# Kernel tuning notes

Hardware: AMD Instinct MI355X
Metric: run time of the kernel (lower is better)

The kernel has to match this reference:

```python
import jax, jax.numpy as jnp
import numpy as np
from jax import lax

DIM = 384
HEADS = 8
HEAD_DIM = DIM // HEADS  # 48
GROUPS = 2               # GKVA num_group
MLP_DIM = 4 * DIM
EPS = 1e-5


def _layernorm(x, g, b):
    m = jnp.mean(x, axis=-1, keepdims=True)
    v = jnp.var(x, axis=-1, keepdims=True)
    return (x - m) * lax.rsqrt(v + EPS) * g + b


def _cpe(x, w, b, dims):
    # depthwise Conv3d positional encoding; x: (B,N,C)
    B, N, C = x.shape
    D, H, W = dims
    feat = jnp.transpose(x.reshape(B, D, H, W, C), (0, 4, 1, 2, 3))  # (B,C,D,H,W)
    feat = lax.conv_general_dilated(
        feat, w, (1, 1, 1), 'SAME',
        dimension_numbers=('NCDHW', 'OIDHW', 'NCDHW'),
        feature_group_count=C)
    feat = feat + b[None, :, None, None, None]
    feat = jnp.transpose(feat, (0, 2, 3, 4, 1)).reshape(B, N, C)
    return x + feat


def _channel_attn_gkva(x, q_w, kv_w, proj_w, proj_b):
    # x: (B,N,C). GKVA: q has num_group heads, kv has full num_heads split into groups.
    B, N, C = x.shape
    scale = HEAD_DIM ** -0.5
    hpg = HEADS // GROUPS  # heads per group = 4
    q = (x @ q_w).reshape(B, 1, N, GROUPS, HEAD_DIM)
    q = jnp.transpose(q, (0, 3, 1, 2, 4))                 # (B,G,1,N,hd)
    kv = (x @ kv_w).reshape(B, N, 2, GROUPS, hpg, HEAD_DIM)
    kv = jnp.transpose(kv, (2, 0, 3, 4, 1, 5))            # (2,B,G,hpg,N,hd)
    k, v = kv[0] * scale, kv[1]
    # channel attention: (hd x hd) score per head, softmax in fp32
    att = jnp.einsum('bghnc,bghnd->bghcd', k, v)          # (B,G,hpg,hd,hd)
    att = jax.nn.softmax(att.astype(jnp.float32), axis=-1).astype(x.dtype)
    y = att @ jnp.swapaxes(q, -1, -2)                     # (B,G,hpg,hd,N) via broadcast over hpg
    y = jnp.swapaxes(y, -1, -2)                           # (B,G,hpg,N,hd)
    y = jnp.transpose(y, (0, 2, 1, 3, 4)).reshape(B, N, C)  # faithful to torch transpose(1,2).reshape
    return y @ proj_w + proj_b


def reference(x, attn_mask, cpe0_w, cpe0_b, cpe1_w, cpe1_b,
              norm1_g, norm1_b, q_w, kv_w, proj_w, proj_b,
              norm2_g, norm2_b, mlp_w1, mlp_b1, mlp_w2, mlp_b2):
    B, D, H, W, C = x.shape
    dims = (D, H, W)
    xf = x.reshape(B, -1, C)
    xf = _cpe(xf, cpe0_w, cpe0_b, dims)
    cur = _channel_attn_gkva(_layernorm(xf, norm1_g, norm1_b), q_w, kv_w, proj_w, proj_b)
    xf = xf + cur  # drop_path = 0 -> identity
    xf = _cpe(xf, cpe1_w, cpe1_b, dims)
    h = _layernorm(xf, norm2_g, norm2_b)
    h = jax.nn.gelu(h @ mlp_w1 + mlp_b1, approximate=False) @ mlp_w2 + mlp_b2
    xf = xf + h
    return xf.reshape(B, D, H, W, C)


def setup_inputs() -> dict:
    key = jax.random.key(0)
    ks = jax.random.split(key, 16)
    B, D, H, W, C = 4, 8, 32, 32, DIM
    s = 0.02
    inp = {
        'x': jax.random.normal(ks[0], (B, D, H, W, C), jnp.float32),
        'attn_mask': jnp.zeros((1, 343, 343), jnp.float32),
        'cpe0_w': jax.random.normal(ks[1], (C, 1, 3, 3, 3), jnp.float32) * s,
        'cpe0_b': jnp.zeros((C,), jnp.float32),
        'cpe1_w': jax.random.normal(ks[2], (C, 1, 3, 3, 3), jnp.float32) * s,
        'cpe1_b': jnp.zeros((C,), jnp.float32),
        'norm1_g': jnp.ones((C,), jnp.float32),
        'norm1_b': jnp.zeros((C,), jnp.float32),
        'q_w': jax.random.normal(ks[3], (C, HEAD_DIM * GROUPS), jnp.float32) * s,
        'kv_w': jax.random.normal(ks[4], (C, 2 * C), jnp.float32) * s,
        'proj_w': jax.random.normal(ks[5], (C, C), jnp.float32) * s,
        'proj_b': jnp.zeros((C,), jnp.float32),
        'norm2_g': jnp.ones((C,), jnp.float32),
        'norm2_b': jnp.zeros((C,), jnp.float32),
        'mlp_w1': jax.random.normal(ks[6], (C, MLP_DIM), jnp.float32) * s,
        'mlp_b1': jnp.zeros((MLP_DIM,), jnp.float32),
        'mlp_w2': jax.random.normal(ks[7], (MLP_DIM, C), jnp.float32) * s,
        'mlp_b2': jnp.zeros((C,), jnp.float32),
    }
    return inp
```

## Files before the change

### kernel.cpp

```cpp
#include <hip/hip_runtime.h>
#include <hip/hip_bf16.h>
#include <math.h>

using bf16 = __hip_bfloat16;
typedef __attribute__((ext_vector_type(8))) short s16x8;
typedef __attribute__((ext_vector_type(4))) float f32x4;

__device__ __forceinline__ float bf2f(unsigned short u) {
    return __uint_as_float(((unsigned int)u) << 16);
}
__device__ __forceinline__ unsigned short f2bf(float f) {
    union { bf16 b; unsigned short u; } cv; cv.b = __float2bfloat16(f); return cv.u;
}
__device__ __forceinline__ float4 ld4(const float* p) { return *(const float4*)p; }
__device__ __forceinline__ float4 ld4(const bf16* p) {
    ushort4 u = *(const ushort4*)p;
    return make_float4(bf2f(u.x), bf2f(u.y), bf2f(u.z), bf2f(u.w));
}

#define GLD16(g, l) __builtin_amdgcn_global_load_lds( \
    (const __attribute__((address_space(1))) unsigned int*)(const void*)(g), \
    (__attribute__((address_space(3))) unsigned int*)(void*)(l), 16, 0, 0)

__device__ __forceinline__ void wtbT(const float* __restrict__ src,
                                     bf16* __restrict__ dst, int K, int N, int i)
{
    int n = i / K, k = i % K;
    dst[i] = (n < N) ? __float2bfloat16(src[k * N + n]) : __float2bfloat16(0.f);
}

__global__ __launch_bounds__(256) void prep_kernel(
    const float* q_w, const float* kv_w, const float* proj_w,
    const float* w1, const float* w2,
    const float* cpe0_w, const float* cpe1_w,
    bf16* qwT, bf16* kvwT, bf16* pwT, bf16* w1T, bf16* w2T,
    float* wt0, float* wt1)
{
    int i = blockIdx.x * 256 + threadIdx.x;
    if      (i < 49152)   wtbT(q_w,    qwT,  384, 96,   i);
    else if (i < 344064)  wtbT(kv_w,   kvwT, 384, 768,  i - 49152);
    else if (i < 491520)  wtbT(proj_w, pwT,  384, 384,  i - 344064);
    else if (i < 1081344) wtbT(w1,     w1T,  384, 1536, i - 491520);
    else if (i < 1671168) wtbT(w2,     w2T,  1536, 384, i - 1081344);
    else if (i < 1681536) { int j = i - 1671168; wt0[(j % 27) * 384 + j / 27] = cpe0_w[j]; }
    else if (i < 1691904) { int j = i - 1681536; wt1[(j % 27) * 384 + j / 27] = cpe1_w[j]; }
}

template <typename T>
__global__ __launch_bounds__(384) void cpe_ln_kernel(
    const T* __restrict__ src, const float* __restrict__ wgtT,
    const float* __restrict__ bias, const float* __restrict__ gam,
    const float* __restrict__ bet, bf16* __restrict__ xf_out,
    bf16* __restrict__ t_out)
{
    const int tid = threadIdx.x;
    const int qd = tid % 96, c = qd * 4;
    const int wseg = tid / 96, w_base = wseg * 8;
    const int blk = blockIdx.x;
    const int h = blk & 31, d = (blk >> 5) & 7, b = blk >> 8;

    const float4 bv = *(const float4*)(bias + c);
    float4 acc[8];
    #pragma unroll
    for (int o = 0; o < 8; ++o) acc[o] = bv;

    #pragma unroll
    for (int kd = 0; kd < 3; ++kd) {
        const int dd = d + kd - 1;
        if ((unsigned)dd >= 8u) continue;
        #pragma unroll
        for (int kh = 0; kh < 3; ++kh) {
            const int hh = h + kh - 1;
            if ((unsigned)hh >= 32u) continue;
            const int tap0 = kd * 9 + kh * 3;
            const float4 w0 = *(const float4*)(wgtT + (tap0 + 0) * 384 + c);
            const float4 w1 = *(const float4*)(wgtT + (tap0 + 1) * 384 + c);
            const float4 w2 = *(const float4*)(wgtT + (tap0 + 2) * 384 + c);
            const T* rowp = src + ((((size_t)b * 8 + dd) * 32 + hh) * 32) * 384 + c;
            #pragma unroll
            for (int p = 0; p < 10; ++p) {
                const int ww = w_base + p - 1;
                const float m = ((unsigned)ww < 32u) ? 1.f : 0.f;
                const int wwc = min(max(ww, 0), 31);
                float4 sv = ld4(rowp + (size_t)wwc * 384);
                sv.x *= m; sv.y *= m; sv.z *= m; sv.w *= m;
                if (p < 8) {
                    acc[p].x += sv.x * w0.x; acc[p].y += sv.y * w0.y;
                    acc[p].z += sv.z * w0.z; acc[p].w += sv.w * w0.w;
                }
                if (p >= 1 && p <= 8) {
                    acc[p-1].x += sv.x * w1.x; acc[p-1].y += sv.y * w1.y;
                    acc[p-1].z += sv.z * w1.z; acc[p-1].w += sv.w * w1.w;
                }
                if (p >= 2) {
                    acc[p-2].x += sv.x * w2.x; acc[p-2].y += sv.y * w2.y;
                    acc[p-2].z += sv.z * w2.z; acc[p-2].w += sv.w * w2.w;
                }
            }
        }
    }
    const size_t rowoff = ((((size_t)b * 8 + d) * 32 + h) * 32) * 384 + c;
    float4 r[8];
    __shared__ float2 part[32][96];
    #pragma unroll
    for (int o = 0; o < 8; ++o) {
        const size_t off = rowoff + (size_t)(w_base + o) * 384;
        const float4 s0 = ld4(src + off);
        r[o].x = s0.x + acc[o].x; r[o].y = s0.y + acc[o].y;
        r[o].z = s0.z + acc[o].z; r[o].w = s0.w + acc[o].w;
        ushort4 u;
        u.x = f2bf(r[o].x); u.y = f2bf(r[o].y); u.z = f2bf(r[o].z); u.w = f2bf(r[o].w);
        *(ushort4*)((unsigned short*)xf_out + off) = u;
        const float s = r[o].x + r[o].y + r[o].z + r[o].w;
        const float s2 = r[o].x*r[o].x + r[o].y*r[o].y + r[o].z*r[o].z + r[o].w*r[o].w;
        part[w_base + o][qd] = make_float2(s, s2);
    }
    __syncthreads();
    __shared__ float2 red[32][12];
    {
        const int tk = tid / 12, j = tid % 12;
        float s = 0.f, s2 = 0.f;
        #pragma unroll
        for (int u = 0; u < 8; ++u) {
            const float2 p = part[tk][j * 8 + u];
            s += p.x; s2 += p.y;
        }
        red[tk][j] = make_float2(s, s2);
    }
    __syncthreads();
    __shared__ float2 stats[32];
    if (tid < 32) {
        float s = 0.f, s2 = 0.f;
        #pragma unroll
        for (int j = 0; j < 12; ++j) { s += red[tid][j].x; s2 += red[tid][j].y; }
        const float mean = s * (1.f / 384.f);
        const float var = s2 * (1.f / 384.f) - mean * mean;
        stats[tid] = make_float2(mean, rsqrtf(var + 1e-5f));
    }
    __syncthreads();
    const float4 gv = *(const float4*)(gam + c);
    const float4 be = *(const float4*)(bet + c);
    #pragma unroll
    for (int o = 0; o < 8; ++o) {
        const int tk = w_base + o;
        const float2 st = stats[tk];
        ushort4 u;
        u.x = f2bf((r[o].x - st.x) * st.y * gv.x + be.x);
        u.y = f2bf((r[o].y - st.x) * st.y * gv.y + be.y);
        u.z = f2bf((r[o].z - st.x) * st.y * gv.z + be.z);
        u.w = f2bf((r[o].w - st.x) * st.y * gv.w + be.w);
        *(ushort4*)((unsigned short*)t_out + (size_t)(blk * 32 + tk) * 384 + c) = u;
    }
}

__global__ __launch_bounds__(256) void gemm128_kernel(
    const bf16* __restrict__ A, int lda,
    const bf16* __restrict__ BT, int ldb,
    void* outp, int ldo, const void* resp, const float* __restrict__ bias,
    int Nout, int K, int flags)
{
    __shared__ unsigned short As[128 * 64];
    __shared__ unsigned short Bs[128 * 64];
    const int tid = threadIdx.x;
    const int wid = tid >> 6, lane = tid & 63;
    const int m0 = blockIdx.y * 128, n0 = blockIdx.x * 128;
    const int moff = (wid >> 1) * 64, noff = (wid & 1) * 64;
    const int lrow = lane & 15, quad = lane >> 4;
    const int srow = lane >> 3;
    const int scol = ((lane & 7) ^ srow) * 8;
    const int sw = lrow & 7;

    f32x4 acc[4][4] = {};

    for (int k0 = 0; k0 < K; k0 += 64) {
        #pragma unroll
        for (int j = 0; j < 4; ++j) {
            const int r = (wid * 4 + j) * 8 + srow;
            GLD16(A + (size_t)(m0 + r) * lda + k0 + scol, As + (wid * 4 + j) * 512);
        }
        #pragma unroll
        for (int j = 0; j < 4; ++j) {
            const int r = (wid * 4 + j) * 8 + srow;
            GLD16(BT + (size_t)(n0 + r) * ldb + k0 + scol, Bs + (wid * 4 + j) * 512);
        }
        __syncthreads();
        #pragma unroll
        for (int ks = 0; ks < 64; ks += 32) {
            const int kc = (ks >> 3) + quad;
            const int koff = ((kc ^ sw) << 3);
            s16x8 af[4], bfr[4];
            #pragma unroll
            for (int i = 0; i < 4; ++i)
                af[i] = *(const s16x8*)(As + (moff + i * 16 + lrow) * 64 + koff);
            #pragma unroll
            for (int i = 0; i < 4; ++i)
                bfr[i] = *(const s16x8*)(Bs + (noff + i * 16 + lrow) * 64 + koff);
            #pragma unroll
            for (int mi = 0; mi < 4; ++mi)
                #pragma unroll
                for (int ni = 0; ni < 4; ++ni)
                    acc[mi][ni] = __builtin_amdgcn_mfma_f32_16x16x32_bf16(
                        af[mi], bfr[ni], acc[mi][ni], 0, 0, 0);
        }
        __syncthreads();
    }

    const bool gelu  = (flags & 1) != 0;
    const bool ofp32 = (flags & 2) != 0;
    const bool rbf16 = (flags & 4) != 0;
    const int rbase = quad * 4;
    #pragma unroll
    for (int mi = 0; mi < 4; ++mi) {
        #pragma unroll
        for (int ni = 0; ni < 4; ++ni) {
            const int gn = n0 + noff + ni * 16 + lrow;
            if (gn >= Nout) continue;
            const float bval = bias ? bias[gn] : 0.f;
            #pragma unroll
            for (int r = 0; r < 4; ++r) {
                const int gm = m0 + moff + mi * 16 + rbase + r;
                const size_t oi = (size_t)gm * ldo + gn;
                float v = acc[mi][ni][r] + bval;
                if (gelu) v = 0.5f * v * (1.f + erff(v * 0.70710678118f));
                if (resp) v += rbf16 ? bf2f(((const unsigned short*)resp)[oi])
                                     : ((const float*)resp)[oi];
                if (ofp32) ((float*)outp)[oi] = v;
                else       ((bf16*)outp)[oi] = __float2bfloat16(v);
            }
        }
    }
}

__global__ __launch_bounds__(64) void attp_kernel(
    const bf16* __restrict__ kvb, float* __restrict__ attp)
{
    const int bgh = blockIdx.x, split = blockIdx.y;
    const int b = bgh >> 3, rr = bgh & 7, g = rr >> 2, h = rr & 3;
    const int kcol = g * 192 + h * 48, vcol = 384 + g * 192 + h * 48;
    __shared__ unsigned short Ks[256 * 48];
    __shared__ unsigned short Vs[256 * 48];
    const int lane = threadIdx.x;

    const size_t rowbase = (size_t)(b * 8192 + split * 256) * 768;
    for (int i = lane; i < 256 * 6; i += 64) {
        const int row = i / 6, part = i % 6;
        const size_t gi = rowbase + (size_t)row * 768;
        *(uint4*)(Ks + row * 48 + part * 8) = *(const uint4*)(kvb + gi + kcol + part * 8);
        *(uint4*)(Vs + row * 48 + part * 8) = *(const uint4*)(kvb + gi + vcol + part * 8);
    }
    __syncthreads();

    f32x4 acc[3][3] = {};
    const int col = lane & 15, kb = (lane >> 4) * 8;
    for (int ks = 0; ks < 256; ks += 32) {
        s16x8 af[3], bfr[3];
        #pragma unroll
        for (int t3 = 0; t3 < 3; ++t3) {
            #pragma unroll
            for (int j = 0; j < 8; ++j) {
                const int tok = ks + kb + j;
                af[t3][j]  = (short)Ks[tok * 48 + t3 * 16 + col];
                bfr[t3][j] = (short)Vs[tok * 48 + t3 * 16 + col];
            }
        }
        #pragma unroll
        for (int ct = 0; ct < 3; ++ct)
            #pragma unroll
            for (int dt = 0; dt < 3; ++dt)
                acc[ct][dt] = __builtin_amdgcn_mfma_f32_16x16x32_bf16(
                    af[ct], bfr[dt], acc[ct][dt], 0, 0, 0);
    }
    const float scale = 0.14433756729740643f;
    float* op = attp + ((size_t)bgh * 32 + split) * 2304;
    const int rbase = (lane >> 4) * 4;
    #pragma unroll
    for (int ct = 0; ct < 3; ++ct)
        #pragma unroll
        for (int dt = 0; dt < 3; ++dt)
            #pragma unroll
            for (int r = 0; r < 4; ++r)
                op[(ct * 16 + rbase + r) * 48 + dt * 16 + col] = scale * acc[ct][dt][r];
}

__global__ __launch_bounds__(256) void attred_kernel(
    const float* __restrict__ attp, bf16* __restrict__ att)
{
    const int bgh = blockIdx.x, tid = threadIdx.x;
    __shared__ float s[2304];
    for (int i = tid; i < 2304; i += 256) {
        float a = 0.f;
        for (int sp = 0; sp < 32; ++sp) a += attp[((size_t)bgh * 32 + sp) * 2304 + i];
        s[i] = a;
    }
    __syncthreads();
    if (tid < 48) {
        const int base = tid * 48;
        float mx = -1e30f;
        for (int d = 0; d < 48; ++d) mx = fmaxf(mx, s[base + d]);
        float sum = 0.f;
        for (int d = 0; d < 48; ++d) sum += expf(s[base + d] - mx);
        float inv = 1.f / sum;
        for (int d = 0; d < 48; ++d)
            att[(size_t)bgh * 2304 + base + d] = __float2bfloat16(expf(s[base + d] - mx) * inv);
    }
}

__global__ __launch_bounds__(256) void y_kernel(
    const bf16* __restrict__ q, const bf16* __restrict__ att, bf16* __restrict__ y)
{
    const int m0 = blockIdx.x * 128;
    const int b = blockIdx.y >> 3, h2g = blockIdx.y & 7;
    const int g = h2g & 1, hh = h2g >> 1;
    const int bgh = b * 8 + g * 4 + hh;
    const int tid = threadIdx.x, wid = tid >> 6, lane = tid & 63;
    __shared__ unsigned short Qs[128 * 64];
    __shared__ unsigned short Ats[48 * 64];

    for (int i = tid; i < 128 * 6; i += 256) {
        const int row = i / 6, part = i % 6;
        *(uint4*)(Qs + row * 64 + part * 8) =
            *(const uint4*)(q + (size_t)(b * 8192 + m0 + row) * 96 + g * 48 + part * 8);
    }
    {
        const int row = tid / 2, half = tid & 1;
        *(uint4*)(Qs + row * 64 + 48 + half * 8) = make_uint4(0, 0, 0, 0);
    }
    for (int i = tid; i < 48 * 6; i += 256) {
        const int row = i / 6, part = i % 6;
        *(uint4*)(Ats + row * 64 + part * 8) =
            *(const uint4*)(att + (size_t)bgh * 2304 + row * 48 + part * 8);
    }
    for (int i = tid; i < 96; i += 256) {
        const int row = i / 2, half = i & 1;
        *(uint4*)(Ats + row * 64 + 48 + half * 8) = make_uint4(0, 0, 0, 0);
    }
    __syncthreads();

    const int moff = wid * 32;
    const int col = lane & 15, kb = (lane >> 4) * 8;
    f32x4 acc[2][3] = {};
    #pragma unroll
    for (int ks = 0; ks < 64; ks += 32) {
        s16x8 af[2], bfr[3];
        #pragma unroll
        for (int mt = 0; mt < 2; ++mt)
            af[mt] = *(const s16x8*)(Qs + (moff + mt * 16 + col) * 64 + ks + kb);
        #pragma unroll
        for (int nt = 0; nt < 3; ++nt)
            bfr[nt] = *(const s16x8*)(Ats + (nt * 16 + col) * 64 + ks + kb);
        #pragma unroll
        for (int mt = 0; mt < 2; ++mt)
            #pragma unroll
            for (int nt = 0; nt < 3; ++nt)
                acc[mt][nt] = __builtin_amdgcn_mfma_f32_16x16x32_bf16(
                    af[mt], bfr[nt], acc[mt][nt], 0, 0, 0);
    }
    const int rbase = (lane >> 4) * 4;
    #pragma unroll
    for (int mt = 0; mt < 2; ++mt) {
        #pragma unroll
        for (int nt = 0; nt < 3; ++nt) {
            const int d = nt * 16 + col;
            #pragma unroll
            for (int r = 0; r < 4; ++r) {
                const int n = m0 + moff + mt * 16 + rbase + r;
                y[((size_t)b * 8192 + h2g * 1024 + (n >> 3)) * 384 + (n & 7) * 48 + d] =
                    __float2bfloat16(acc[mt][nt][r]);
            }
        }
    }
}

extern "C" void kernel_launch(void* const* d_in, const int* in_sizes, int n_in,
                              void* d_out, int out_size, void* d_ws, size_t ws_size,
                              hipStream_t stream)
{
    (void)in_sizes; (void)n_in; (void)out_size; (void)ws_size;
    const float* x      = (const float*)d_in[0];
    const float* cpe0_w = (const float*)d_in[2];
    const float* cpe0_b = (const float*)d_in[3];
    const float* cpe1_w = (const float*)d_in[4];
    const float* cpe1_b = (const float*)d_in[5];
    const float* n1g    = (const float*)d_in[6];
    const float* n1b    = (const float*)d_in[7];
    const float* q_w    = (const float*)d_in[8];
    const float* kv_w   = (const float*)d_in[9];
    const float* proj_w = (const float*)d_in[10];
    const float* proj_b = (const float*)d_in[11];
    const float* n2g    = (const float*)d_in[12];
    const float* n2b    = (const float*)d_in[13];
    const float* w1     = (const float*)d_in[14];
    const float* b1     = (const float*)d_in[15];
    const float* w2     = (const float*)d_in[16];
    const float* b2     = (const float*)d_in[17];

    char* ws = (char*)d_ws;
    bf16*  qwT  = (bf16*)(ws + 0);
    bf16*  kvwT = (bf16*)(ws + 98304);
    bf16*  pwT  = (bf16*)(ws + 688128);
    bf16*  w1T  = (bf16*)(ws + 983040);
    bf16*  w2T  = (bf16*)(ws + 2162688);
    float* wt0  = (float*)(ws + 3342336);
    float* wt1  = (float*)(ws + 3383808);
    bf16*  xf   = (bf16*)(ws + 4194304);
    bf16*  qb   = (bf16*)(ws + 29360128);
    float* attp = (float*)(ws + 35651584);
    bf16*  att  = (bf16*)(ws + 45088768);
    bf16*  yb   = (bf16*)(ws + 46137344);
    bf16*  h1   = (bf16*)(ws + 4194304);
    bf16*  t    = (bf16*)(ws + 104857600);
    bf16*  kv   = (bf16*)(ws + 130023424);
    bf16*  xf3  = (bf16*)(ws + 130023424);

    prep_kernel<<<dim3(6609), dim3(256), 0, stream>>>(
        q_w, kv_w, proj_w, w1, w2, cpe0_w, cpe1_w,
        qwT, kvwT, pwT, w1T, w2T, wt0, wt1);

    cpe_ln_kernel<float><<<dim3(1024), dim3(384), 0, stream>>>(
        x, wt0, cpe0_b, n1g, n1b, xf, t);
    gemm128_kernel<<<dim3(1, 256), dim3(256), 0, stream>>>(
        t, 384, qwT, 384, qb, 96, nullptr, nullptr, 96, 384, 0);
    gemm128_kernel<<<dim3(6, 256), dim3(256), 0, stream>>>(
        t, 384, kvwT, 384, kv, 768, nullptr, nullptr, 768, 384, 0);
    attp_kernel<<<dim3(32, 32), dim3(64), 0, stream>>>(kv, attp);
    attred_kernel<<<dim3(32), dim3(256), 0, stream>>>(attp, att);
    y_kernel<<<dim3(64, 32), dim3(256), 0, stream>>>(qb, att, yb);
    gemm128_kernel<<<dim3(3, 256), dim3(256), 0, stream>>>(
        yb, 384, pwT, 384, xf, 384, xf, proj_b, 384, 384, 4);
    cpe_ln_kernel<bf16><<<dim3(1024), dim3(384), 0, stream>>>(
        xf, wt1, cpe1_b, n2g, n2b, xf3, t);
    gemm128_kernel<<<dim3(12, 256), dim3(256), 0, stream>>>(
        t, 384, w1T, 384, h1, 1536, nullptr, b1, 1536, 384, 1);
    gemm128_kernel<<<dim3(3, 256), dim3(256), 0, stream>>>(
        h1, 1536, w2T, 1536, d_out, 384, xf3, b2, 384, 1536, 2 | 4);
}
```

Baseline: 548.1 us.

## Fuse Q and KV projections into one GEMM, swap grid order, fast GELU

Merges the Q and KV weight matrices into a single padded 896-column transposed weight, so one GEMM produces q, k and v together and the activation tile is read once instead of twice. It also swaps the GEMM grid so blockIdx.x walks M tiles, which changes the order in which blocks share weight and activation tiles in cache. The third change replaces erff in the GELU epilogue with an Abramowitz-Stegun polynomial using a fast reciprocal and exp. The polynomial is accurate to roughly 1e-7 absolute, and the padding adds 32 wasted zero columns of compute.

New measurement: 526.2 us. 1.04x faster.

```diff
diff --git a/kernel.cpp b/kernel.cpp
--- a/kernel.cpp
+++ b/kernel.cpp
@@ -18,6 +18,20 @@
     return make_float4(bf2f(u.x), bf2f(u.y), bf2f(u.z), bf2f(u.w));
 }
 
+__device__ __forceinline__ float gelu_f(float v) {
+    const float x = 0.70710678118f * v;
+    const float ax = fabsf(x);
+    const float t = __builtin_amdgcn_rcpf(fmaf(0.3275911f, ax, 1.f));
+    float p = fmaf(1.061405429f, t, -1.453152027f);
+    p = fmaf(p, t, 1.421413741f);
+    p = fmaf(p, t, -0.284496736f);
+    p = fmaf(p, t, 0.254829592f);
+    p *= t;
+    const float e = __expf(-x * x);
+    const float er = copysignf(fmaf(-p, e, 1.f), x);
+    return 0.5f * v * (1.f + er);
+}
+
 #define GLD16(g, l) __builtin_amdgcn_global_load_lds( \
     (const __attribute__((address_space(1))) unsigned int*)(const void*)(g), \
     (__attribute__((address_space(3))) unsigned int*)(void*)(l), 16, 0, 0)
@@ -33,12 +47,17 @@
     const float* q_w, const float* kv_w, const float* proj_w,
     const float* w1, const float* w2,
     const float* cpe0_w, const float* cpe1_w,
-    bf16* qwT, bf16* kvwT, bf16* pwT, bf16* w1T, bf16* w2T,
+    bf16* qkvT, bf16* pwT, bf16* w1T, bf16* w2T,
     float* wt0, float* wt1)
 {
     int i = blockIdx.x * 256 + threadIdx.x;
-    if      (i < 49152)   wtbT(q_w,    qwT,  384, 96,   i);
-    else if (i < 344064)  wtbT(kv_w,   kvwT, 384, 768,  i - 49152);
+    if (i < 344064) {
+        int n = i / 384, k = i % 384;
+        float v = 0.f;
+        if (n < 96)       v = q_w[k * 96 + n];
+        else if (n >= 128) v = kv_w[k * 768 + (n - 128)];
+        qkvT[i] = __float2bfloat16(v);
+    }
     else if (i < 491520)  wtbT(proj_w, pwT,  384, 384,  i - 344064);
     else if (i < 1081344) wtbT(w1,     w1T,  384, 1536, i - 491520);
     else if (i < 1671168) wtbT(w2,     w2T,  1536, 384, i - 1081344);
@@ -163,7 +182,7 @@
     __shared__ unsigned short Bs[128 * 64];
     const int tid = threadIdx.x;
     const int wid = tid >> 6, lane = tid & 63;
-    const int m0 = blockIdx.y * 128, n0 = blockIdx.x * 128;
+    const int m0 = blockIdx.x * 128, n0 = blockIdx.y * 128;
     const int moff = (wid >> 1) * 64, noff = (wid & 1) * 64;
     const int lrow = lane & 15, quad = lane >> 4;
     const int srow = lane >> 3;
@@ -221,7 +240,7 @@
                 const int gm = m0 + moff + mi * 16 + rbase + r;
                 const size_t oi = (size_t)gm * ldo + gn;
                 float v = acc[mi][ni][r] + bval;
-                if (gelu) v = 0.5f * v * (1.f + erff(v * 0.70710678118f));
+                if (gelu) v = gelu_f(v);
                 if (resp) v += rbf16 ? bf2f(((const unsigned short*)resp)[oi])
                                      : ((const float*)resp)[oi];
                 if (ofp32) ((float*)outp)[oi] = v;
@@ -232,21 +251,21 @@
 }
 
 __global__ __launch_bounds__(64) void attp_kernel(
-    const bf16* __restrict__ kvb, float* __restrict__ attp)
+    const bf16* __restrict__ qkv, float* __restrict__ attp)
 {
     const int bgh = blockIdx.x, split = blockIdx.y;
     const int b = bgh >> 3, rr = bgh & 7, g = rr >> 2, h = rr & 3;
-    const int kcol = g * 192 + h * 48, vcol = 384 + g * 192 + h * 48;
+    const int kcol = 128 + g * 192 + h * 48, vcol = 512 + g * 192 + h * 48;
     __shared__ unsigned short Ks[256 * 48];
     __shared__ unsigned short Vs[256 * 48];
     const int lane = threadIdx.x;
 
-    const size_t rowbase = (size_t)(b * 8192 + split * 256) * 768;
+    const size_t rowbase = (size_t)(b * 8192 + split * 256) * 896;
     for (int i = lane; i < 256 * 6; i += 64) {
         const int row = i / 6, part = i % 6;
-        const size_t gi = rowbase + (size_t)row * 768;
-        *(uint4*)(Ks + row * 48 + part * 8) = *(const uint4*)(kvb + gi + kcol + part * 8);
-        *(uint4*)(Vs + row * 48 + part * 8) = *(const uint4*)(kvb + gi + vcol + part * 8);
+        const size_t gi = rowbase + (size_t)row * 896;
+        *(uint4*)(Ks + row * 48 + part * 8) = *(const uint4*)(qkv + gi + kcol + part * 8);
+        *(uint4*)(Vs + row * 48 + part * 8) = *(const uint4*)(qkv + gi + vcol + part * 8);
     }
     __syncthreads();
 
@@ -306,7 +325,7 @@
 }
 
 __global__ __launch_bounds__(256) void y_kernel(
-    const bf16* __restrict__ q, const bf16* __restrict__ att, bf16* __restrict__ y)
+    const bf16* __restrict__ qkv, const bf16* __restrict__ att, bf16* __restrict__ y)
 {
     const int m0 = blockIdx.x * 128;
     const int b = blockIdx.y >> 3, h2g = blockIdx.y & 7;
@@ -319,7 +338,7 @@
     for (int i = tid; i < 128 * 6; i += 256) {
         const int row = i / 6, part = i % 6;
         *(uint4*)(Qs + row * 64 + part * 8) =
-            *(const uint4*)(q + (size_t)(b * 8192 + m0 + row) * 96 + g * 48 + part * 8);
+            *(const uint4*)(qkv + (size_t)(b * 8192 + m0 + row) * 896 + g * 48 + part * 8);
     }
     {
         const int row = tid / 2, half = tid & 1;
@@ -395,42 +414,38 @@
     const float* b2     = (const float*)d_in[17];
 
     char* ws = (char*)d_ws;
-    bf16*  qwT  = (bf16*)(ws + 0);
-    bf16*  kvwT = (bf16*)(ws + 98304);
+    bf16*  qkvT = (bf16*)(ws + 0);
     bf16*  pwT  = (bf16*)(ws + 688128);
     bf16*  w1T  = (bf16*)(ws + 983040);
     bf16*  w2T  = (bf16*)(ws + 2162688);
     float* wt0  = (float*)(ws + 3342336);
     float* wt1  = (float*)(ws + 3383808);
     bf16*  xf   = (bf16*)(ws + 4194304);
-    bf16*  qb   = (bf16*)(ws + 29360128);
-    float* attp = (float*)(ws + 35651584);
-    bf16*  att  = (bf16*)(ws + 45088768);
-    bf16*  yb   = (bf16*)(ws + 46137344);
+    bf16*  qkv  = (bf16*)(ws + 29360128);
+    float* attp = (float*)(ws + 88080384);
+    bf16*  att  = (bf16*)(ws + 97517568);
+    bf16*  yb   = (bf16*)(ws + 98566144);
+    bf16*  t    = (bf16*)(ws + 123731968);
+    bf16*  xf3  = (bf16*)(ws + 148897792);
     bf16*  h1   = (bf16*)(ws + 4194304);
-    bf16*  t    = (bf16*)(ws + 104857600);
-    bf16*  kv   = (bf16*)(ws + 130023424);
-    bf16*  xf3  = (bf16*)(ws + 130023424);
 
     prep_kernel<<<dim3(6609), dim3(256), 0, stream>>>(
         q_w, kv_w, proj_w, w1, w2, cpe0_w, cpe1_w,
-        qwT, kvwT, pwT, w1T, w2T, wt0, wt1);
+        qkvT, pwT, w1T, w2T, wt0, wt1);
 
     cpe_ln_kernel<float><<<dim3(1024), dim3(384), 0, stream>>>(
         x, wt0, cpe0_b, n1g, n1b, xf, t);
-    gemm128_kernel<<<dim3(1, 256), dim3(256), 0, stream>>>(
-        t, 384, qwT, 384, qb, 96, nullptr, nullptr, 96, 384, 0);
-    gemm128_kernel<<<dim3(6, 256), dim3(256), 0, stream>>>(
-        t, 384, kvwT, 384, kv, 768, nullptr, nullptr, 768, 384, 0);
-    attp_kernel<<<dim3(32, 32), dim3(64), 0, stream>>>(kv, attp);
+    gemm128_kernel<<<dim3(256, 7), dim3(256), 0, stream>>>(
+        t, 384, qkvT, 384, qkv, 896, nullptr, nullptr, 896, 384, 0);
+    attp_kernel<<<dim3(32, 32), dim3(64), 0, stream>>>(qkv, attp);
     attred_kernel<<<dim3(32), dim3(256), 0, stream>>>(attp, att);
-    y_kernel<<<dim3(64, 32), dim3(256), 0, stream>>>(qb, att, yb);
-    gemm128_kernel<<<dim3(3, 256), dim3(256), 0, stream>>>(
+    y_kernel<<<dim3(64, 32), dim3(256), 0, stream>>>(qkv, att, yb);
+    gemm128_kernel<<<dim3(256, 3), dim3(256), 0, stream>>>(
         yb, 384, pwT, 384, xf, 384, xf, proj_b, 384, 384, 4);
     cpe_ln_kernel<bf16><<<dim3(1024), dim3(384), 0, stream>>>(
         xf, wt1, cpe1_b, n2g, n2b, xf3, t);
-    gemm128_kernel<<<dim3(12, 256), dim3(256), 0, stream>>>(
+    gemm128_kernel<<<dim3(256, 12), dim3(256), 0, stream>>>(
         t, 384, w1T, 384, h1, 1536, nullptr, b1, 1536, 384, 1);
-    gemm128_kernel<<<dim3(3, 256), dim3(256), 0, stream>>>(
+    gemm128_kernel<<<dim3(256, 3), dim3(256), 0, stream>>>(
         h1, 1536, w2T, 1536, d_out, 384, xf3, b2, 384, 1536, 2 | 4);
 }
```
